# Optimization experiments

Hardware: AMD Instinct MI355X
Metric: run time of the kernel (lower is better)

The kernel has to match this reference:

```python
import jax, jax.numpy as jnp
import numpy as np

N = 50000        # num_nodes
E = 800000       # num_edges (avg degree 16)
K = 3            # Chebyshev order
F_IN = 144       # 144 * in_channels
F_OUT = 144      # 144 * out_channels


def setup_inputs() -> dict:
    key = jax.random.key(0)
    k1, k2, k3, k4, k5 = jax.random.split(key, 5)
    x = jax.random.normal(k1, (N, F_IN), dtype=jnp.float32)
    edge_index = jax.random.randint(k2, (2, E), 0, N, dtype=jnp.int32)
    edge_weight = jax.random.uniform(k3, (E,), dtype=jnp.float32)
    weight = jax.random.normal(k4, (K, F_IN, F_OUT), dtype=jnp.float32) * 0.02
    bias = jax.random.normal(k5, (F_OUT,), dtype=jnp.float32) * 0.02
    return {"x": x, "edge_index": edge_index, "edge_weight": edge_weight,
            "weight": weight, "bias": bias}


def reference(x, edge_index, edge_weight, weight, bias):
    row, col = edge_index[0], edge_index[1]
    # remove_self_loops: mask out edges with row == col (fixed-shape equivalent)
    mask = (row != col).astype(x.dtype)
    w = edge_weight * mask
    # degree over remaining edges, deg^-0.5 with inf -> 0
    deg = jax.ops.segment_sum(mask, row, num_segments=N)
    dinv = jnp.where(deg > 0, deg ** -0.5, jnp.zeros_like(deg))
    lap = -dinv[row] * w * dinv[col]  # [E]

    def spmm(v):  # out[i] = sum_{e: row_e = i} lap_e * v[col_e]
        return jax.ops.segment_sum(lap[:, None] * v[col], row, num_segments=N)

    Tx0 = x
    out = Tx0 @ weight[0]
    Tx1 = spmm(Tx0)
    out = out + Tx1 @ weight[1]
    for k in range(2, weight.shape[0]):
        Tx2 = 2.0 * spmm(Tx1) - Tx0
        out = out + Tx2 @ weight[k]
        Tx0, Tx1 = Tx1, Tx2
    return out + bias
```

## Files before the change

### kernel.cpp

```cpp
#include <hip/hip_runtime.h>
#include <hip/hip_bf16.h>

#define NN 50000
#define EE 800000
#define FF 144
#define CVTBLK 1758
#define ECHK 2048
#define NBE 391
#define NBKT_REAL 391
#define NBUCKET 392
#define WGRID 284
#define HM (NBUCKET * NBE)
#define SCANBLK 599

typedef __hip_bfloat16 bf16;
typedef __attribute__((ext_vector_type(8))) short short8;
typedef __attribute__((ext_vector_type(4))) float floatx4;
typedef __attribute__((ext_vector_type(2))) float float2v;

__device__ inline float blo(unsigned x) { return __uint_as_float(x << 16); }
__device__ inline float bhi(unsigned x) { return __uint_as_float(x & 0xffff0000u); }

__device__ inline void dec4fma(float* a, float l, unsigned d) {
    float2v p0 = __builtin_amdgcn_cvt_pk_f32_fp8((int)d, false);
    float2v p1 = __builtin_amdgcn_cvt_pk_f32_fp8((int)d, true);
    a[0] = fmaf(l, p0.x, a[0]);
    a[1] = fmaf(l, p0.y, a[1]);
    a[2] = fmaf(l, p1.x, a[2]);
    a[3] = fmaf(l, p1.y, a[3]);
}
__device__ inline void fma16q(float* a, float l, uint4 u) {
    dec4fma(a + 0, l, u.x);
    dec4fma(a + 4, l, u.y);
    dec4fma(a + 8, l, u.z);
    dec4fma(a + 12, l, u.w);
}
__device__ inline unsigned enc4(float a, float b, float c, float d) {
    int w = __builtin_amdgcn_cvt_pk_fp8_f32(a, b, 0, false);
    w = __builtin_amdgcn_cvt_pk_fp8_f32(c, d, w, true);
    return (unsigned)w;
}

__device__ inline void load_edge(const int* ei, int e, int flag, int& r, int& c) {
    if (flag) { r = ei[2 * e]; c = ei[2 * EE + 2 * e]; }
    else      { r = ei[e];     c = ei[EE + e]; }
}


__global__ void fusedA_k(const float* __restrict__ x, bf16* __restrict__ xb,
                         unsigned char* __restrict__ xq,
                         const int* __restrict__ ei, const float* __restrict__ ew,
                         unsigned long long* __restrict__ items, int* __restrict__ hist,
                         const float* __restrict__ wt, short* __restrict__ wtb) {
    __shared__ int lh[NBUCKET];
    __shared__ int nzf;
    int b = blockIdx.x;
    int tid = threadIdx.x;
    if (b < CVTBLK) {
        int t = b * 256 + tid;
        if (t >= NN * FF / 16) return;
        const float4* xp = (const float4*)x + t * 4;
        float4 v0 = xp[0], v1 = xp[1], v2 = xp[2], v3 = xp[3];
        float f[16] = {v0.x, v0.y, v0.z, v0.w, v1.x, v1.y, v1.z, v1.w,
                       v2.x, v2.y, v2.z, v2.w, v3.x, v3.y, v3.z, v3.w};
        unsigned short hs[16];
        #pragma unroll
        for (int j = 0; j < 16; ++j) {
            bf16 bb = (bf16)f[j];
            hs[j] = *(unsigned short*)&bb;
        }
        uint4* xbq = (uint4*)xb + t * 2;
        xbq[0] = ((uint4*)hs)[0];
        xbq[1] = ((uint4*)hs)[1];
        uint4 q;
        q.x = enc4(f[0], f[1], f[2], f[3]);
        q.y = enc4(f[4], f[5], f[6], f[7]);
        q.z = enc4(f[8], f[9], f[10], f[11]);
        q.w = enc4(f[12], f[13], f[14], f[15]);
        ((uint4*)xq)[t] = q;
    } else if (b < CVTBLK + NBE) {
        int bb = b - CVTBLK;
        if (tid == 0) nzf = 0;
        for (int j = tid; j < NBUCKET; j += 256) lh[j] = 0;
        __syncthreads();
        int eb = bb * ECHK;
        unsigned acc = 0;
        #pragma unroll
        for (int k = 0; k < ECHK / 256; ++k) {
            int e = eb + k * 256 + tid;
            if (e < EE) acc |= (unsigned)ei[2 * e + 1];
        }
        if (acc) nzf = 1;
        __syncthreads();
        int flag = (nzf == 0) ? 1 : 0;
        #pragma unroll
        for (int k = 0; k < ECHK / 256; ++k) {
            int e = eb + k * 256 + tid;
            if (e < EE) {
                int r, c; load_edge(ei, e, flag, r, c);
                unsigned key = (r == c) ? 0xFFFFu : (unsigned)r;
                items[e] = ((unsigned long long)((key << 16) | (unsigned)c) << 32)
                           | (unsigned long long)__float_as_uint(ew[e]);
                atomicAdd(&lh[min(key >> 7, (unsigned)NBKT_REAL)], 1);
            }
        }
        __syncthreads();
        for (int j = tid; j < NBUCKET; j += 256) hist[j * NBE + bb] = lh[j];
    } else {
        int t = (b - CVTBLK - NBE) * 256 + tid;
        if (t >= 3 * FF * 168) return;
        int ph = t / (FF * 168);
        int rem = t - ph * FF * 168;
        int o = rem / 168;
        int i = rem - o * 168;
        short v = 0;
        if (i < FF) {
            float fv;
            if (ph == 0)      fv = wt[i * FF + o] - wt[2 * FF * FF + i * FF + o];
            else if (ph == 1) fv = wt[FF * FF + i * FF + o];
            else              fv = 2.0f * wt[2 * FF * FF + i * FF + o];
            bf16 bv = (bf16)fv;
            v = *(const short*)&bv;
        }
        wtb[t] = v;
    }
}


__global__ void scanA1_k(int* __restrict__ hist, int* __restrict__ bsumA) {
    __shared__ int wsum[4], woff[4];
    int b = blockIdx.x, tid = threadIdx.x;
    int wv = tid >> 6, ln = tid & 63;
    int i = b * 256 + tid;
    int v = (i < HM) ? hist[i] : 0;
    int xs = v;
    #pragma unroll
    for (int off = 1; off < 64; off <<= 1) {
        int t = __shfl_up(xs, off, 64);
        if (ln >= off) xs += t;
    }
    if (ln == 63) wsum[wv] = xs;
    __syncthreads();
    if (tid == 0) {
        int s = 0;
        #pragma unroll
        for (int j = 0; j < 4; ++j) { woff[j] = s; s += wsum[j]; }
        bsumA[b] = s;
    }
    __syncthreads();
    if (i < HM) hist[i] = woff[wv] + (xs - v);
}

__global__ __launch_bounds__(1024) void scanA2_k(int* __restrict__ bsumA) {
    __shared__ int wsum[16], woff[16];
    int tid = threadIdx.x, wv = tid >> 6, ln = tid & 63;
    int v = (tid < SCANBLK) ? bsumA[tid] : 0;
    int xs = v;
    #pragma unroll
    for (int off = 1; off < 64; off <<= 1) {
        int t = __shfl_up(xs, off, 64);
        if (ln >= off) xs += t;
    }
    if (ln == 63) wsum[wv] = xs;
    __syncthreads();
    if (tid == 0) {
        int s = 0;
        #pragma unroll
        for (int j = 0; j < 16; ++j) { woff[j] = s; s += wsum[j]; }
    }
    __syncthreads();
    if (tid < SCANBLK) bsumA[tid] = woff[wv] + (xs - v);
}

__device__ inline int hbase(const int* hist, const int* bsumA, int f) {
    return hist[f] + bsumA[f >> 8];
}


__global__ void pscat_k(const unsigned long long* __restrict__ items,
                        const int* __restrict__ hist, const int* __restrict__ bsumA,
                        unsigned long long* __restrict__ sorted) {
    __shared__ int lbase[NBUCKET];
    int b = blockIdx.x, tid = threadIdx.x;
    for (int j = tid; j < NBUCKET; j += 256) {
        int f = j * NBE + b;
        lbase[j] = hbase(hist, bsumA, f);
    }
    __syncthreads();
    int eb = b * ECHK;
    #pragma unroll
    for (int k = 0; k < ECHK / 256; ++k) {
        int e = eb + k * 256 + tid;
        if (e < EE) {
            unsigned long long it = items[e];
            unsigned key = (unsigned)(it >> 48);
            int bk = (int)min(key >> 7, (unsigned)NBKT_REAL);
            int slot = atomicAdd(&lbase[bk], 1);
            sorted[slot] = it;
        }
    }
}


__global__ void fine1_k(const unsigned long long* __restrict__ sorted,
                        const int* __restrict__ hist, const int* __restrict__ bsumA,
                        int* __restrict__ rowptr, float* __restrict__ dinv) {
    __shared__ int lh[128];
    __shared__ int wtot;
    int b = blockIdx.x, tid = threadIdx.x;
    if (tid < 128) lh[tid] = 0;
    int s = hbase(hist, bsumA, b * NBE);
    int e = hbase(hist, bsumA, (b + 1) * NBE);
    __syncthreads();
    for (int p = s + tid; p < e; p += 256)
        atomicAdd(&lh[(int)(unsigned)(sorted[p] >> 48) - b * 128], 1);
    __syncthreads();
    int ln = tid & 63;
    int v = (tid < 128) ? lh[tid] : 0;
    int xs = v;
    #pragma unroll
    for (int off = 1; off < 64; off <<= 1) {
        int t = __shfl_up(xs, off, 64);
        if (ln >= off) xs += t;
    }
    if (tid == 63) wtot = xs;
    __syncthreads();
    int excl = xs - v + ((tid >= 64 && tid < 128) ? wtot : 0);
    int gr = b * 128 + tid;
    if (tid < 128 && gr < NN) {
        rowptr[gr] = s + excl;
        dinv[gr] = v > 0 ? rsqrtf((float)v) : 0.f;
    }
    if (b == NBKT_REAL - 1 && tid == 0) rowptr[NN] = e;
}


__global__ void fine2_k(const unsigned long long* __restrict__ sorted,
                        const int* __restrict__ hist, const int* __restrict__ bsumA,
                        const int* __restrict__ rowptr, const float* __restrict__ dinv,
                        unsigned* __restrict__ pairs) {
    __shared__ int lrp[128];
    __shared__ float ldv[128];
    int b = blockIdx.x, tid = threadIdx.x;
    int gr = b * 128 + tid;
    if (tid < 128) {
        lrp[tid] = (gr < NN) ? rowptr[gr] : 0;
        ldv[tid] = (gr < NN) ? dinv[gr] : 0.f;
    }
    int s = hbase(hist, bsumA, b * NBE);
    int e = hbase(hist, bsumA, (b + 1) * NBE);
    __syncthreads();
    for (int p = s + tid; p < e; p += 256) {
        unsigned long long it = sorted[p];
        int lr = (int)(unsigned)(it >> 48) - b * 128;
        unsigned c = (unsigned)(it >> 32) & 0xFFFFu;
        float w = __uint_as_float((unsigned)it);
        float lap = -ldv[lr] * dinv[c] * w;
        int slot = atomicAdd(&lrp[lr], 1);
        bf16 lb = (bf16)lap;
        pairs[slot] = c | ((unsigned)*(unsigned short*)&lb << 16);
    }
}


template <int WRITEQ>
__global__ void spmm_k(const unsigned char* __restrict__ vq,
                       const int* __restrict__ rowptr, const unsigned* __restrict__ pairs,
                       bf16* __restrict__ y, unsigned char* __restrict__ yq) {
    int t = blockIdx.x * 256 + threadIdx.x;
    if (t >= NN * 9) return;
    int i = t / 9;
    int fo = (t - i * 9) * 16;
    const unsigned char* vp = vq + fo;

    float a[16];
    #pragma unroll
    for (int j = 0; j < 16; ++j) a[j] = 0.f;

    int s = rowptr[i], e = rowptr[i + 1];
    int p = s;
    for (; p + 1 < e; p += 2) {
        unsigned pr0 = pairs[p], pr1 = pairs[p + 1];
        uint4 u0 = *(const uint4*)(vp + (pr0 & 0xffffu) * FF);
        uint4 u1 = *(const uint4*)(vp + (pr1 & 0xffffu) * FF);
        fma16q(a, bhi(pr0), u0);
        fma16q(a, bhi(pr1), u1);
    }
    if (p < e) {
        unsigned pr = pairs[p];
        uint4 u = *(const uint4*)(vp + (pr & 0xffffu) * FF);
        fma16q(a, bhi(pr), u);
    }

    unsigned short hs[16];
    #pragma unroll
    for (int j = 0; j < 16; ++j) {
        bf16 b = (bf16)a[j];
        hs[j] = *(unsigned short*)&b;
    }
    uint4* yp = (uint4*)((unsigned short*)y + i * FF + fo);
    yp[0] = ((uint4*)hs)[0];
    yp[1] = ((uint4*)hs)[1];

    if (WRITEQ) {
        uint4 q;
        q.x = enc4(a[0], a[1], a[2], a[3]);
        q.y = enc4(a[4], a[5], a[6], a[7]);
        q.z = enc4(a[8], a[9], a[10], a[11]);
        q.w = enc4(a[12], a[13], a[14], a[15]);
        *(uint4*)(yq + i * FF + fo) = q;
    }
}


__global__ __launch_bounds__(1024)
void gemm_fused(const bf16* __restrict__ A0, const bf16* __restrict__ A1,
                const bf16* __restrict__ A2, const short* __restrict__ wtb,
                const float* __restrict__ bias, float* __restrict__ out) {
    __shared__ __align__(16) short Wt[3 * 144 * 168];
    int tid = threadIdx.x;

    {
        const uint4* Wg = (const uint4*)wtb;
        uint4* Wl = (uint4*)Wt;
        #pragma unroll
        for (int q = 0; q < 9; ++q) {
            int idx = q * 1024 + tid;
            if (idx < 9072) Wl[idx] = Wg[idx];
        }
    }
    __syncthreads();

    int wv = tid >> 6, ln = tid & 63;
    int m16 = ln & 15, quad = ln >> 4;
    int tile = wv * 256 + blockIdx.x;
    if (tile * 16 >= NN) return;
    int rowBase = tile * 16;
    int row = rowBase + m16;

    const bf16* const srcs[3] = {A0, A1, A2};
    const short8 zero8 = {0, 0, 0, 0, 0, 0, 0, 0};

    floatx4 acc[9];
    #pragma unroll
    for (int q = 0; q < 9; ++q) acc[q] = (floatx4){0.f, 0.f, 0.f, 0.f};

    #pragma unroll
    for (int ph = 0; ph < 3; ++ph) {
        const bf16* A = srcs[ph];
        short8 a[5];
        #pragma unroll
        for (int kt = 0; kt < 5; ++kt) {
            int k0 = kt * 32 + quad * 8;
            if (k0 < FF)
                a[kt] = *(const short8*)((const short*)A + row * FF + k0);
            else
                a[kt] = zero8;
        }

        const short* Wp = Wt + ph * 144 * 168;
        #pragma unroll
        for (int nt = 0; nt < 9; ++nt) {
            #pragma unroll
            for (int kt = 0; kt < 5; ++kt) {
                short8 b = *(const short8*)&Wp[(nt * 16 + m16) * 168 + kt * 32 + quad * 8];
                acc[nt] = __builtin_amdgcn_mfma_f32_16x16x32_bf16(a[kt], b, acc[nt], 0, 0, 0);
            }
        }
    }

    int rowc = rowBase + quad * 4;
    #pragma unroll
    for (int nt = 0; nt < 9; ++nt) {
        int col = nt * 16 + m16;
        float bs = bias[col];
        #pragma unroll
        for (int r = 0; r < 4; ++r) {
            int rr = rowc + r;
            out[rr * FF + col] = acc[nt][r] + bs;
        }
    }
}


extern "C" void kernel_launch(void* const* d_in, const int* in_sizes, int n_in,
                              void* d_out, int out_size, void* d_ws, size_t ws_size,
                              hipStream_t stream) {
    int ix = -1, iei = -1, iew = -1, iwt = -1, ib = -1;
    for (int i = 0; i < n_in; ++i) {
        switch (in_sizes[i]) {
            case NN * FF:      if (ix  < 0) ix  = i; break;
            case 2 * EE:       if (iei < 0) iei = i; break;
            case EE:           if (iew < 0) iew = i; break;
            case 3 * FF * FF:  if (iwt < 0) iwt = i; break;
            case FF:           if (ib  < 0) ib  = i; break;
        }
    }
    if (ix < 0 || iei < 0 || iew < 0 || iwt < 0 || ib < 0) {
        ix = 0; iei = 1; iew = 2; iwt = 3; ib = 4;
    }
    const float* x    = (const float*)d_in[ix];
    const int*   ei   = (const int*)d_in[iei];
    const float* ew   = (const float*)d_in[iew];
    const float* wt   = (const float*)d_in[iwt];
    const float* bias = (const float*)d_in[ib];
    float* out = (float*)d_out;

    char* p = (char*)d_ws;
    unsigned long long* items  = (unsigned long long*)(p + 0);
    unsigned long long* sorted = (unsigned long long*)(p + 6400000);
    int*      hist   = (int*)(p + 12800000);
    int*      bsumA  = (int*)(p + 13500000);
    int*      rowptr = (int*)(p + 13600000);
    float*    dinv   = (float*)(p + 13900000);
    unsigned* pairs  = (unsigned*)(p + 14200000);
    short*    wtb    = (short*)(p + 17500000);
    bf16*     tx1    = (bf16*)(p + 17700000);
    bf16*     tx2    = (bf16*)(p + 32100000);
    unsigned char* xq   = (unsigned char*)(p + 46500000);
    unsigned char* tx1q = (unsigned char*)(p + 53700000);
    bf16*     xb     = (bf16*)(p + 60900000);

    if (ws_size < 75300000) return;

    int spGrid = (NN * 9 + 255) / 256;

    fusedA_k<<<CVTBLK + NBE + WGRID, 256, 0, stream>>>(x, xb, xq, ei, ew, items, hist,
                                                       wt, wtb);
    scanA1_k<<<SCANBLK, 256, 0, stream>>>(hist, bsumA);
    scanA2_k<<<1, 1024, 0, stream>>>(bsumA);
    pscat_k<<<NBE, 256, 0, stream>>>(items, hist, bsumA, sorted);
    fine1_k<<<NBKT_REAL, 256, 0, stream>>>(sorted, hist, bsumA, rowptr, dinv);
    fine2_k<<<NBKT_REAL, 256, 0, stream>>>(sorted, hist, bsumA, rowptr, dinv, pairs);

    spmm_k<1><<<spGrid, 256, 0, stream>>>(xq, rowptr, pairs, tx1, tx1q);
    spmm_k<0><<<spGrid, 256, 0, stream>>>(tx1q, rowptr, pairs, tx2, (unsigned char*)0);
    gemm_fused<<<256, 1024, 0, stream>>>(xb, tx1, tx2, wtb, bias, out);
}
```

Baseline: 190.3 us.

## Fuse preprocessing and SpMM stages into one cooperative persistent kernel

Replaces eight separate kernel launches (conversion, histogram scan, scatter, fine sort, two SpMMs) with a single cooperative kernel of 1536 blocks that uses grid-wide syncs between phases and grid-stride loops over virtual blocks. The aim is to remove per-launch overhead and inter-kernel gaps. It also rewrites the second-level scan to use 256 threads with three elements each. The cost is lower parallelism per phase (fixed grid, occupancy capped at 6 blocks/CU), grid.sync overhead, and a fallback path if cooperative launch is unavailable.

```diff
diff --git a/kernel.cpp b/kernel.cpp
--- a/kernel.cpp
+++ b/kernel.cpp
@@ -1,5 +1,8 @@
 #include <hip/hip_runtime.h>
 #include <hip/hip_bf16.h>
+#include <hip/hip_cooperative_groups.h>
+
+namespace cg = cooperative_groups;
 
 #define NN 50000
 #define EE 800000
@@ -12,6 +15,9 @@
 #define WGRID 284
 #define HM (NBUCKET * NBE)
 #define SCANBLK 599
+#define SPBLK 1758
+#define NV0 (CVTBLK + NBE + WGRID)
+#define MGRID 1536
 
 typedef __hip_bfloat16 bf16;
 typedef __attribute__((ext_vector_type(8))) short short8;
@@ -47,89 +53,85 @@
 }
 
 
-__global__ void fusedA_k(const float* __restrict__ x, bf16* __restrict__ xb,
-                         unsigned char* __restrict__ xq,
-                         const int* __restrict__ ei, const float* __restrict__ ew,
-                         unsigned long long* __restrict__ items, int* __restrict__ hist,
-                         const float* __restrict__ wt, short* __restrict__ wtb) {
-    __shared__ int lh[NBUCKET];
-    __shared__ int nzf;
-    int b = blockIdx.x;
-    int tid = threadIdx.x;
-    if (b < CVTBLK) {
-        int t = b * 256 + tid;
-        if (t >= NN * FF / 16) return;
-        const float4* xp = (const float4*)x + t * 4;
-        float4 v0 = xp[0], v1 = xp[1], v2 = xp[2], v3 = xp[3];
-        float f[16] = {v0.x, v0.y, v0.z, v0.w, v1.x, v1.y, v1.z, v1.w,
-                       v2.x, v2.y, v2.z, v2.w, v3.x, v3.y, v3.z, v3.w};
-        unsigned short hs[16];
-        #pragma unroll
-        for (int j = 0; j < 16; ++j) {
-            bf16 bb = (bf16)f[j];
-            hs[j] = *(unsigned short*)&bb;
-        }
-        uint4* xbq = (uint4*)xb + t * 2;
-        xbq[0] = ((uint4*)hs)[0];
-        xbq[1] = ((uint4*)hs)[1];
-        uint4 q;
-        q.x = enc4(f[0], f[1], f[2], f[3]);
-        q.y = enc4(f[4], f[5], f[6], f[7]);
-        q.z = enc4(f[8], f[9], f[10], f[11]);
-        q.w = enc4(f[12], f[13], f[14], f[15]);
-        ((uint4*)xq)[t] = q;
-    } else if (b < CVTBLK + NBE) {
-        int bb = b - CVTBLK;
-        if (tid == 0) nzf = 0;
-        for (int j = tid; j < NBUCKET; j += 256) lh[j] = 0;
-        __syncthreads();
-        int eb = bb * ECHK;
-        unsigned acc = 0;
-        #pragma unroll
-        for (int k = 0; k < ECHK / 256; ++k) {
-            int e = eb + k * 256 + tid;
-            if (e < EE) acc |= (unsigned)ei[2 * e + 1];
-        }
-        if (acc) nzf = 1;
-        __syncthreads();
-        int flag = (nzf == 0) ? 1 : 0;
-        #pragma unroll
-        for (int k = 0; k < ECHK / 256; ++k) {
-            int e = eb + k * 256 + tid;
-            if (e < EE) {
-                int r, c; load_edge(ei, e, flag, r, c);
-                unsigned key = (r == c) ? 0xFFFFu : (unsigned)r;
-                items[e] = ((unsigned long long)((key << 16) | (unsigned)c) << 32)
-                           | (unsigned long long)__float_as_uint(ew[e]);
-                atomicAdd(&lh[min(key >> 7, (unsigned)NBKT_REAL)], 1);
-            }
-        }
-        __syncthreads();
-        for (int j = tid; j < NBUCKET; j += 256) hist[j * NBE + bb] = lh[j];
-    } else {
-        int t = (b - CVTBLK - NBE) * 256 + tid;
-        if (t >= 3 * FF * 168) return;
-        int ph = t / (FF * 168);
-        int rem = t - ph * FF * 168;
-        int o = rem / 168;
-        int i = rem - o * 168;
-        short v = 0;
-        if (i < FF) {
-            float fv;
-            if (ph == 0)      fv = wt[i * FF + o] - wt[2 * FF * FF + i * FF + o];
-            else if (ph == 1) fv = wt[FF * FF + i * FF + o];
-            else              fv = 2.0f * wt[2 * FF * FF + i * FF + o];
-            bf16 bv = (bf16)fv;
-            v = *(const short*)&bv;
-        }
-        wtb[t] = v;
-    }
-}
-
-
-__global__ void scanA1_k(int* __restrict__ hist, int* __restrict__ bsumA) {
-    __shared__ int wsum[4], woff[4];
-    int b = blockIdx.x, tid = threadIdx.x;
+__device__ inline void dev_cvt(int b, int tid, const float* __restrict__ x,
+                               bf16* __restrict__ xb, unsigned char* __restrict__ xq) {
+    int t = b * 256 + tid;
+    if (t >= NN * FF / 16) return;
+    const float4* xp = (const float4*)x + t * 4;
+    float4 v0 = xp[0], v1 = xp[1], v2 = xp[2], v3 = xp[3];
+    float f[16] = {v0.x, v0.y, v0.z, v0.w, v1.x, v1.y, v1.z, v1.w,
+                   v2.x, v2.y, v2.z, v2.w, v3.x, v3.y, v3.z, v3.w};
+    unsigned short hs[16];
+    #pragma unroll
+    for (int j = 0; j < 16; ++j) {
+        bf16 bb = (bf16)f[j];
+        hs[j] = *(unsigned short*)&bb;
+    }
+    uint4* xbq = (uint4*)xb + t * 2;
+    xbq[0] = ((uint4*)hs)[0];
+    xbq[1] = ((uint4*)hs)[1];
+    uint4 q;
+    q.x = enc4(f[0], f[1], f[2], f[3]);
+    q.y = enc4(f[4], f[5], f[6], f[7]);
+    q.z = enc4(f[8], f[9], f[10], f[11]);
+    q.w = enc4(f[12], f[13], f[14], f[15]);
+    ((uint4*)xq)[t] = q;
+}
+
+__device__ inline void dev_edge(int bb, int tid, const int* __restrict__ ei,
+                                const float* __restrict__ ew,
+                                unsigned long long* __restrict__ items,
+                                int* __restrict__ hist, int* lh, int* nzf) {
+    if (tid == 0) *nzf = 0;
+    for (int j = tid; j < NBUCKET; j += 256) lh[j] = 0;
+    __syncthreads();
+    int eb = bb * ECHK;
+    unsigned acc = 0;
+    #pragma unroll
+    for (int k = 0; k < ECHK / 256; ++k) {
+        int e = eb + k * 256 + tid;
+        if (e < EE) acc |= (unsigned)ei[2 * e + 1];
+    }
+    if (acc) *nzf = 1;
+    __syncthreads();
+    int flag = (*nzf == 0) ? 1 : 0;
+    #pragma unroll
+    for (int k = 0; k < ECHK / 256; ++k) {
+        int e = eb + k * 256 + tid;
+        if (e < EE) {
+            int r, c; load_edge(ei, e, flag, r, c);
+            unsigned key = (r == c) ? 0xFFFFu : (unsigned)r;
+            items[e] = ((unsigned long long)((key << 16) | (unsigned)c) << 32)
+                       | (unsigned long long)__float_as_uint(ew[e]);
+            atomicAdd(&lh[min(key >> 7, (unsigned)NBKT_REAL)], 1);
+        }
+    }
+    __syncthreads();
+    for (int j = tid; j < NBUCKET; j += 256) hist[j * NBE + bb] = lh[j];
+}
+
+__device__ inline void dev_cvtw(int b, int tid, const float* __restrict__ wt,
+                                short* __restrict__ wtb) {
+    int t = b * 256 + tid;
+    if (t >= 3 * FF * 168) return;
+    int ph = t / (FF * 168);
+    int rem = t - ph * FF * 168;
+    int o = rem / 168;
+    int i = rem - o * 168;
+    short v = 0;
+    if (i < FF) {
+        float fv;
+        if (ph == 0)      fv = wt[i * FF + o] - wt[2 * FF * FF + i * FF + o];
+        else if (ph == 1) fv = wt[FF * FF + i * FF + o];
+        else              fv = 2.0f * wt[2 * FF * FF + i * FF + o];
+        bf16 bv = (bf16)fv;
+        v = *(const short*)&bv;
+    }
+    wtb[t] = v;
+}
+
+__device__ inline void dev_scanA1(int b, int tid, int* __restrict__ hist,
+                                  int* __restrict__ bsumA, int* wsum, int* woff) {
     int wv = tid >> 6, ln = tid & 63;
     int i = b * 256 + tid;
     int v = (i < HM) ? hist[i] : 0;
@@ -151,11 +153,14 @@
     if (i < HM) hist[i] = woff[wv] + (xs - v);
 }
 
-__global__ __launch_bounds__(1024) void scanA2_k(int* __restrict__ bsumA) {
-    __shared__ int wsum[16], woff[16];
-    int tid = threadIdx.x, wv = tid >> 6, ln = tid & 63;
-    int v = (tid < SCANBLK) ? bsumA[tid] : 0;
-    int xs = v;
+__device__ inline void dev_scanA2(int tid, int* __restrict__ bsumA, int* wsum, int* woff) {
+    int wv = tid >> 6, ln = tid & 63;
+    int j0 = tid * 3;
+    int v0 = (j0 < SCANBLK) ? bsumA[j0] : 0;
+    int v1 = (j0 + 1 < SCANBLK) ? bsumA[j0 + 1] : 0;
+    int v2 = (j0 + 2 < SCANBLK) ? bsumA[j0 + 2] : 0;
+    int sv = v0 + v1 + v2;
+    int xs = sv;
     #pragma unroll
     for (int off = 1; off < 64; off <<= 1) {
         int t = __shfl_up(xs, off, 64);
@@ -166,26 +171,23 @@
     if (tid == 0) {
         int s = 0;
         #pragma unroll
-        for (int j = 0; j < 16; ++j) { woff[j] = s; s += wsum[j]; }
-    }
-    __syncthreads();
-    if (tid < SCANBLK) bsumA[tid] = woff[wv] + (xs - v);
+        for (int j = 0; j < 4; ++j) { woff[j] = s; s += wsum[j]; }
+    }
+    __syncthreads();
+    int o = woff[wv] + (xs - sv);
+    if (j0 < SCANBLK) bsumA[j0] = o;
+    if (j0 + 1 < SCANBLK) bsumA[j0 + 1] = o + v0;
+    if (j0 + 2 < SCANBLK) bsumA[j0 + 2] = o + v0 + v1;
 }
 
 __device__ inline int hbase(const int* hist, const int* bsumA, int f) {
     return hist[f] + bsumA[f >> 8];
 }
 
-
-__global__ void pscat_k(const unsigned long long* __restrict__ items,
-                        const int* __restrict__ hist, const int* __restrict__ bsumA,
-                        unsigned long long* __restrict__ sorted) {
-    __shared__ int lbase[NBUCKET];
-    int b = blockIdx.x, tid = threadIdx.x;
-    for (int j = tid; j < NBUCKET; j += 256) {
-        int f = j * NBE + b;
-        lbase[j] = hbase(hist, bsumA, f);
-    }
+__device__ inline void dev_pscat(int b, int tid, const unsigned long long* __restrict__ items,
+                                 const int* __restrict__ hist, const int* __restrict__ bsumA,
+                                 unsigned long long* __restrict__ sorted, int* lbase) {
+    for (int j = tid; j < NBUCKET; j += 256) lbase[j] = hbase(hist, bsumA, j * NBE + b);
     __syncthreads();
     int eb = b * ECHK;
     #pragma unroll
@@ -201,31 +203,28 @@
     }
 }
 
-
-__global__ void fine1_k(const unsigned long long* __restrict__ sorted,
-                        const int* __restrict__ hist, const int* __restrict__ bsumA,
-                        int* __restrict__ rowptr, float* __restrict__ dinv) {
-    __shared__ int lh[128];
-    __shared__ int wtot;
-    int b = blockIdx.x, tid = threadIdx.x;
-    if (tid < 128) lh[tid] = 0;
+__device__ inline void dev_fine1(int b, int tid, const unsigned long long* __restrict__ sorted,
+                                 const int* __restrict__ hist, const int* __restrict__ bsumA,
+                                 int* __restrict__ rowptr, float* __restrict__ dinv,
+                                 int* lh128, int* wtot) {
+    if (tid < 128) lh128[tid] = 0;
     int s = hbase(hist, bsumA, b * NBE);
     int e = hbase(hist, bsumA, (b + 1) * NBE);
     __syncthreads();
     for (int p = s + tid; p < e; p += 256)
-        atomicAdd(&lh[(int)(unsigned)(sorted[p] >> 48) - b * 128], 1);
+        atomicAdd(&lh128[(int)(unsigned)(sorted[p] >> 48) - b * 128], 1);
     __syncthreads();
     int ln = tid & 63;
-    int v = (tid < 128) ? lh[tid] : 0;
+    int v = (tid < 128) ? lh128[tid] : 0;
     int xs = v;
     #pragma unroll
     for (int off = 1; off < 64; off <<= 1) {
         int t = __shfl_up(xs, off, 64);
         if (ln >= off) xs += t;
     }
-    if (tid == 63) wtot = xs;
-    __syncthreads();
-    int excl = xs - v + ((tid >= 64 && tid < 128) ? wtot : 0);
+    if (tid == 63) *wtot = xs;
+    __syncthreads();
+    int excl = xs - v + ((tid >= 64 && tid < 128) ? *wtot : 0);
     int gr = b * 128 + tid;
     if (tid < 128 && gr < NN) {
         rowptr[gr] = s + excl;
@@ -234,14 +233,10 @@
     if (b == NBKT_REAL - 1 && tid == 0) rowptr[NN] = e;
 }
 
-
-__global__ void fine2_k(const unsigned long long* __restrict__ sorted,
-                        const int* __restrict__ hist, const int* __restrict__ bsumA,
-                        const int* __restrict__ rowptr, const float* __restrict__ dinv,
-                        unsigned* __restrict__ pairs) {
-    __shared__ int lrp[128];
-    __shared__ float ldv[128];
-    int b = blockIdx.x, tid = threadIdx.x;
+__device__ inline void dev_fine2(int b, int tid, const unsigned long long* __restrict__ sorted,
+                                 const int* __restrict__ hist, const int* __restrict__ bsumA,
+                                 const int* __restrict__ rowptr, const float* __restrict__ dinv,
+                                 unsigned* __restrict__ pairs, int* lrp, float* ldv) {
     int gr = b * 128 + tid;
     if (tid < 128) {
         lrp[tid] = (gr < NN) ? rowptr[gr] : 0;
@@ -262,13 +257,10 @@
     }
 }
 
-
 template <int WRITEQ>
-__global__ void spmm_k(const unsigned char* __restrict__ vq,
-                       const int* __restrict__ rowptr, const unsigned* __restrict__ pairs,
-                       bf16* __restrict__ y, unsigned char* __restrict__ yq) {
-    int t = blockIdx.x * 256 + threadIdx.x;
-    if (t >= NN * 9) return;
+__device__ inline void dev_spmm(int t, const unsigned char* __restrict__ vq,
+                                const int* __restrict__ rowptr, const unsigned* __restrict__ pairs,
+                                bf16* __restrict__ y, unsigned char* __restrict__ yq) {
     int i = t / 9;
     int fo = (t - i * 9) * 16;
     const unsigned char* vp = vq + fo;
@@ -310,6 +302,108 @@
         q.w = enc4(a[12], a[13], a[14], a[15]);
         *(uint4*)(yq + i * FF + fo) = q;
     }
+}
+
+
+__global__ __launch_bounds__(256, 6)
+void mega_k(const float* __restrict__ x, bf16* __restrict__ xb, unsigned char* __restrict__ xq,
+            const int* __restrict__ ei, const float* __restrict__ ew,
+            unsigned long long* __restrict__ items, int* __restrict__ hist,
+            int* __restrict__ bsumA, const float* __restrict__ wt, short* __restrict__ wtb,
+            unsigned long long* __restrict__ sorted, int* __restrict__ rowptr,
+            float* __restrict__ dinv, unsigned* __restrict__ pairs,
+            bf16* __restrict__ tx1, unsigned char* __restrict__ tx1q, bf16* __restrict__ tx2) {
+    __shared__ int lh[NBUCKET];
+    __shared__ int s128[128];
+    __shared__ float f128[128];
+    __shared__ int wsum[4], woff[4];
+    __shared__ int wtot, nzf;
+    cg::grid_group grid = cg::this_grid();
+    int tid = threadIdx.x;
+    int bid = blockIdx.x;
+
+    for (int vb = bid; vb < NV0; vb += MGRID) {
+        if (vb < CVTBLK)            dev_cvt(vb, tid, x, xb, xq);
+        else if (vb < CVTBLK + NBE) dev_edge(vb - CVTBLK, tid, ei, ew, items, hist, lh, &nzf);
+        else                        dev_cvtw(vb - CVTBLK - NBE, tid, wt, wtb);
+    }
+    grid.sync();
+    if (bid < SCANBLK) dev_scanA1(bid, tid, hist, bsumA, wsum, woff);
+    grid.sync();
+    if (bid == 0) dev_scanA2(tid, bsumA, wsum, woff);
+    grid.sync();
+    if (bid < NBE) dev_pscat(bid, tid, items, hist, bsumA, sorted, lh);
+    grid.sync();
+    if (bid < NBKT_REAL) dev_fine1(bid, tid, sorted, hist, bsumA, rowptr, dinv, s128, &wtot);
+    grid.sync();
+    if (bid < NBKT_REAL) dev_fine2(bid, tid, sorted, hist, bsumA, rowptr, dinv, pairs, s128, f128);
+    grid.sync();
+    for (int vb = bid; vb < SPBLK; vb += MGRID) {
+        int t = vb * 256 + tid;
+        if (t < NN * 9) dev_spmm<1>(t, xq, rowptr, pairs, tx1, tx1q);
+    }
+    grid.sync();
+    for (int vb = bid; vb < SPBLK; vb += MGRID) {
+        int t = vb * 256 + tid;
+        if (t < NN * 9) dev_spmm<0>(t, tx1q, rowptr, pairs, tx2, (unsigned char*)0);
+    }
+}
+
+
+__global__ void fusedA_k(const float* __restrict__ x, bf16* __restrict__ xb,
+                         unsigned char* __restrict__ xq,
+                         const int* __restrict__ ei, const float* __restrict__ ew,
+                         unsigned long long* __restrict__ items, int* __restrict__ hist,
+                         const float* __restrict__ wt, short* __restrict__ wtb) {
+    __shared__ int lh[NBUCKET];
+    __shared__ int nzf;
+    int b = blockIdx.x, tid = threadIdx.x;
+    if (b < CVTBLK)            dev_cvt(b, tid, x, xb, xq);
+    else if (b < CVTBLK + NBE) dev_edge(b - CVTBLK, tid, ei, ew, items, hist, lh, &nzf);
+    else                       dev_cvtw(b - CVTBLK - NBE, tid, wt, wtb);
+}
+
+__global__ void scanA1_k(int* __restrict__ hist, int* __restrict__ bsumA) {
+    __shared__ int wsum[4], woff[4];
+    dev_scanA1(blockIdx.x, threadIdx.x, hist, bsumA, wsum, woff);
+}
+
+__global__ void scanA2_k(int* __restrict__ bsumA) {
+    __shared__ int wsum[4], woff[4];
+    dev_scanA2(threadIdx.x, bsumA, wsum, woff);
+}
+
+__global__ void pscat_k(const unsigned long long* __restrict__ items,
+                        const int* __restrict__ hist, const int* __restrict__ bsumA,
+                        unsigned long long* __restrict__ sorted) {
+    __shared__ int lbase[NBUCKET];
+    dev_pscat(blockIdx.x, threadIdx.x, items, hist, bsumA, sorted, lbase);
+}
+
+__global__ void fine1_k(const unsigned long long* __restrict__ sorted,
+                        const int* __restrict__ hist, const int* __restrict__ bsumA,
+                        int* __restrict__ rowptr, float* __restrict__ dinv) {
+    __shared__ int lh128[128];
+    __shared__ int wtot;
+    dev_fine1(blockIdx.x, threadIdx.x, sorted, hist, bsumA, rowptr, dinv, lh128, &wtot);
+}
+
+__global__ void fine2_k(const unsigned long long* __restrict__ sorted,
+                        const int* __restrict__ hist, const int* __restrict__ bsumA,
+                        const int* __restrict__ rowptr, const float* __restrict__ dinv,
+                        unsigned* __restrict__ pairs) {
+    __shared__ int lrp[128];
+    __shared__ float ldv[128];
+    dev_fine2(blockIdx.x, threadIdx.x, sorted, hist, bsumA, rowptr, dinv, pairs, lrp, ldv);
+}
+
+template <int WRITEQ>
+__global__ void spmm_k(const unsigned char* __restrict__ vq,
+                       const int* __restrict__ rowptr, const unsigned* __restrict__ pairs,
+                       bf16* __restrict__ y, unsigned char* __restrict__ yq) {
+    int t = blockIdx.x * 256 + threadIdx.x;
+    if (t >= NN * 9) return;
+    dev_spmm<WRITEQ>(t, vq, rowptr, pairs, y, yq);
 }
 
 
@@ -423,17 +517,35 @@
 
     if (ws_size < 75300000) return;
 
-    int spGrid = (NN * 9 + 255) / 256;
-
-    fusedA_k<<<CVTBLK + NBE + WGRID, 256, 0, stream>>>(x, xb, xq, ei, ew, items, hist,
-                                                       wt, wtb);
-    scanA1_k<<<SCANBLK, 256, 0, stream>>>(hist, bsumA);
-    scanA2_k<<<1, 1024, 0, stream>>>(bsumA);
-    pscat_k<<<NBE, 256, 0, stream>>>(items, hist, bsumA, sorted);
-    fine1_k<<<NBKT_REAL, 256, 0, stream>>>(sorted, hist, bsumA, rowptr, dinv);
-    fine2_k<<<NBKT_REAL, 256, 0, stream>>>(sorted, hist, bsumA, rowptr, dinv, pairs);
-
-    spmm_k<1><<<spGrid, 256, 0, stream>>>(xq, rowptr, pairs, tx1, tx1q);
-    spmm_k<0><<<spGrid, 256, 0, stream>>>(tx1q, rowptr, pairs, tx2, (unsigned char*)0);
+    static int s_coop = -1;
+    if (s_coop < 0) {
+        int nb = 0;
+        hipError_t oe = hipOccupancyMaxActiveBlocksPerMultiprocessor(&nb, mega_k, 256, 0);
+        s_coop = (oe == hipSuccess && nb >= MGRID / 256) ? 1 : 0;
+    }
+
+    int launched = 0;
+    if (s_coop) {
+        void* args[] = {(void*)&x, (void*)&xb, (void*)&xq, (void*)&ei, (void*)&ew,
+                        (void*)&items, (void*)&hist, (void*)&bsumA, (void*)&wt, (void*)&wtb,
+                        (void*)&sorted, (void*)&rowptr, (void*)&dinv, (void*)&pairs,
+                        (void*)&tx1, (void*)&tx1q, (void*)&tx2};
+        hipError_t e = hipLaunchCooperativeKernel(mega_k, dim3(MGRID), dim3(256),
+                                                  args, 0, stream);
+        if (e == hipSuccess) launched = 1;
+        else s_coop = 0;
+    }
+    if (!launched) {
+        int spGrid = (NN * 9 + 255) / 256;
+        fusedA_k<<<NV0, 256, 0, stream>>>(x, xb, xq, ei, ew, items, hist, wt, wtb);
+        scanA1_k<<<SCANBLK, 256, 0, stream>>>(hist, bsumA);
+        scanA2_k<<<1, 256, 0, stream>>>(bsumA);
+        pscat_k<<<NBE, 256, 0, stream>>>(items, hist, bsumA, sorted);
+        fine1_k<<<NBKT_REAL, 256, 0, stream>>>(sorted, hist, bsumA, rowptr, dinv);
+        fine2_k<<<NBKT_REAL, 256, 0, stream>>>(sorted, hist, bsumA, rowptr, dinv, pairs);
+        spmm_k<1><<<spGrid, 256, 0, stream>>>(xq, rowptr, pairs, tx1, tx1q);
+        spmm_k<0><<<spGrid, 256, 0, stream>>>(tx1q, rowptr, pairs, tx2, (unsigned char*)0);
+    }
+
     gemm_fused<<<256, 1024, 0, stream>>>(xb, tx1, tx2, wtb, bias, out);
 }
```

Result: no change. 186.8 us (-1.8%).
